# Kernel tuning notes

Measured on AMD Instinct MI355X. Metric: run time of the kernel, lower is better.

## Reference

```python
import jax, jax.numpy as jnp
import numpy as np

GROUPS = 16
N_HEADS = 4
EPS = 1e-6


def setup_inputs() -> dict:
    key = jax.random.key(0)
    ks = jax.random.split(key, 7)
    N, C, D, H, W = 2, 256, 16, 16, 16
    x = jax.random.normal(ks[0], (N, C, D, H, W), jnp.float32)
    gn_scale = 1.0 + 0.02 * jax.random.normal(ks[1], (C,), jnp.float32)
    gn_bias = 0.02 * jax.random.normal(ks[2], (C,), jnp.float32)
    w_qkv = jax.random.normal(ks[3], (3 * C, C), jnp.float32) / np.sqrt(C).astype(np.float32)
    b_qkv = 0.02 * jax.random.normal(ks[4], (3 * C,), jnp.float32)
    # NOTE: original zero-inits w_out/b_out (zero_module); we use random values
    # so the kernel-correctness baseline is non-trivial. Same math.
    w_out = jax.random.normal(ks[5], (C, C), jnp.float32) / np.sqrt(C).astype(np.float32)
    b_out = 0.02 * jax.random.normal(ks[6], (C,), jnp.float32)
    return {"x": x, "gn_scale": gn_scale, "gn_bias": gn_bias,
            "w_qkv": w_qkv, "b_qkv": b_qkv, "w_out": w_out, "b_out": b_out}


def reference(x, gn_scale, gn_bias, w_qkv, b_qkv, w_out, b_out):
    N, C, D, H, W = x.shape
    L = D * H * W
    xf = x.reshape(N, C, L)
    # GroupNorm(16 groups, eps=1e-6, affine)
    xg = xf.reshape(N, GROUPS, C // GROUPS, L)
    mu = xg.mean(axis=(2, 3), keepdims=True)
    var = xg.var(axis=(2, 3), keepdims=True)
    xn = ((xg - mu) * jax.lax.rsqrt(var + EPS)).reshape(N, C, L)
    xn = xn * gn_scale[None, :, None] + gn_bias[None, :, None]
    # 1x1x1 Conv3d == channel matmul
    qkv = jnp.einsum('oc,ncl->nol', w_qkv, xn) + b_qkv[None, :, None]  # [N,3C,L]
    ch = C // N_HEADS
    qkv = qkv.reshape(N, 3, N_HEADS, ch, L)  # channel layout: (qkvs, head, ch)
    q, k, v = qkv[:, 0], qkv[:, 1], qkv[:, 2]  # each [N,heads,ch,L]
    scale = 1.0 / np.sqrt(np.sqrt(ch)).astype(np.float32)
    w = jnp.einsum('nhct,nhcs->nhts', q * scale, k * scale)  # [N,heads,L,L]
    w = jax.nn.softmax(w, axis=-1)
    a = jnp.einsum('nhts,nhcs->nhct', w, v).reshape(N, C, L)
    y = jnp.einsum('oc,ncl->nol', w_out, a) + b_out[None, :, None]
    return x + y.reshape(N, C, D, H, W)
```

## Files before the change

### kernel.cpp

```cpp
#include <hip/hip_runtime.h>

#define NB 2
#define CCH 256
#define LL 4096
#define NGRP 16
#define NHD 4
#define CHD 64
#define QR 768
#define SPLIT 4
#define TBLK 256

typedef __attribute__((ext_vector_type(8))) short short8;
typedef __attribute__((ext_vector_type(4))) float f32x4;
typedef __attribute__((ext_vector_type(4))) unsigned int uint32x4;

#define OFF_GP 64
#define OFF_BP 4224
#define OFF_WQ 5824
#define OFF_WO 202432
#define OFF_QT 235200
#define OFF_KT 1283776
#define OFF_V  2332352
#define OFF_PO 3380928
#define OFF_L  7575232
#define OFF_XT OFF_PO
#define OFF_AT OFF_QT

#define KSCALE 0.1803368801111204f

__device__ __forceinline__ unsigned short f2bf(float f) {
    unsigned int u = __builtin_bit_cast(unsigned int, f);
    u += 0x7fffu + ((u >> 16) & 1u);
    return (unsigned short)(u >> 16);
}
__device__ __forceinline__ float bf2f(unsigned short s) {
    unsigned int u = ((unsigned int)s) << 16;
    return __builtin_bit_cast(float, u);
}
__device__ __forceinline__ unsigned int cvtpk(float lo, float hi) {
    unsigned int r;
    asm("v_cvt_pk_bf16_f32 %0, %1, %2" : "=v"(r) : "v"(lo), "v"(hi));
    return r;
}

__device__ __forceinline__ void barrier_lds_only() {
    asm volatile("s_waitcnt lgkmcnt(0)" ::: "memory");
    __builtin_amdgcn_s_barrier();
    __builtin_amdgcn_sched_barrier(0);
}

__device__ __forceinline__ short8 build_pf(const f32x4 s_lo, const f32x4 s_hi) {
    unsigned int a0 = cvtpk(s_lo[0], s_lo[1]);
    unsigned int b0 = cvtpk(s_hi[0], s_hi[1]);
    unsigned int a1 = cvtpk(s_lo[2], s_lo[3]);
    unsigned int b1 = cvtpk(s_hi[2], s_hi[3]);
    asm("v_permlane32_swap_b32 %0, %1" : "+v"(a0), "+v"(b0));
    asm("v_permlane16_swap_b32 %0, %1" : "+v"(a0), "+v"(b0));
    asm("v_permlane32_swap_b32 %0, %1" : "+v"(a1), "+v"(b1));
    asm("v_permlane16_swap_b32 %0, %1" : "+v"(a1), "+v"(b1));
    uint32x4 w = {a0, a1, b0, b1};
    return __builtin_bit_cast(short8, w);
}

__device__ __forceinline__ void stage_tile(unsigned short* lt,
                                           const unsigned short* src,
                                           int srcStride, int tid) {
    #pragma unroll
    for (int p = 0; p < 4; p++) {
        const int r  = p * 16 + (tid >> 4);
        const int cb = (tid & 15) * 2;
        const unsigned short* s = src + (size_t)r * srcStride + cb * 8;
        short8 a = *(const short8*)(s);
        short8 b = *(const short8*)(s + 8);
        char* d = (char*)lt + r * 512;
        *(short8*)(d + (((cb    ) ^ (r & 15)) << 4)) = a;
        *(short8*)(d + (((cb + 1) ^ (r & 15)) << 4)) = b;
    }
}
__device__ __forceinline__ short8 ldsfrag(const unsigned short* lt, int row, int ch) {
    return *(const short8*)((const char*)lt + row * 512 + ((ch ^ (row & 15)) << 4));
}

__global__ __launch_bounds__(256)
void k_xtgn(const float* __restrict__ x, unsigned short* __restrict__ xt,
            float* __restrict__ ws) {
    const int l0 = blockIdx.x * 64, c0 = blockIdx.y * 64, n = blockIdx.z;
    __shared__ __align__(16) unsigned short lt[64 * 64];
    __shared__ float red[2][4][4];
    const int tid = threadIdx.x;
    const int cl = tid >> 4;
    const int ll = (tid & 15) << 2;
    float s1[4], s2[4];
    #pragma unroll
    for (int cc = 0; cc < 4; cc++) {
        const int c = cl + cc * 16;
        float4 v = *(const float4*)(x + (size_t)(n * CCH + c0 + c) * LL + l0 + ll);
        s1[cc] = (v.x + v.y) + (v.z + v.w);
        s2[cc] = (v.x * v.x + v.y * v.y) + (v.z * v.z + v.w * v.w);
        const float vv[4] = {v.x, v.y, v.z, v.w};
        #pragma unroll
        for (int j = 0; j < 4; j++) {
            const int l = ll + j;
            const int byte = l * 128 + ((((c >> 3) ^ (l & 7)) << 4) | ((c & 7) * 2));
            *(unsigned short*)((char*)lt + byte) = f2bf(vv[j]);
        }
    }
    #pragma unroll
    for (int cc = 0; cc < 4; cc++)
        #pragma unroll
        for (int off = 32; off; off >>= 1) {
            s1[cc] += __shfl_down(s1[cc], off);
            s2[cc] += __shfl_down(s2[cc], off);
        }
    if ((tid & 63) == 0) {
        const int w = tid >> 6;
        #pragma unroll
        for (int cc = 0; cc < 4; cc++) { red[0][w][cc] = s1[cc]; red[1][w][cc] = s2[cc]; }
    }
    __syncthreads();
    if (tid < 4) {
        const float a = red[0][0][tid] + red[0][1][tid] + red[0][2][tid] + red[0][3][tid];
        const float b = red[1][0][tid] + red[1][1][tid] + red[1][2][tid] + red[1][3][tid];
        const int g = n * NGRP + (c0 >> 4) + tid;
        ws[OFF_GP + (g * 64 + blockIdx.x) * 2]     = a;
        ws[OFF_GP + (g * 64 + blockIdx.x) * 2 + 1] = b;
    }
    const int lr = tid >> 2;
    const int ch = (tid & 3) << 4;
    unsigned short* dst = xt + ((size_t)n * LL + l0 + lr) * CCH + c0 + ch;
    const int b0 = lr * 128 + ((((ch >> 3)    ) ^ (lr & 7)) << 4);
    const int b1 = lr * 128 + ((((ch >> 3) + 1) ^ (lr & 7)) << 4);
    *(short8*)dst       = *(const short8*)((char*)lt + b0);
    *(short8*)(dst + 8) = *(const short8*)((char*)lt + b1);
}

__device__ __forceinline__ void load_stats(const float* __restrict__ ws,
                                           float* smu, float* srs) {
    if (threadIdx.x < 32) {
        float s1 = 0.f, s2 = 0.f;
        #pragma unroll 8
        for (int i = 0; i < 64; i++) {
            s1 += ws[OFF_GP + (threadIdx.x * 64 + i) * 2];
            s2 += ws[OFF_GP + (threadIdx.x * 64 + i) * 2 + 1];
        }
        const float inv = 1.f / (float)(16 * LL);
        float m = s1 * inv;
        float var = s2 * inv - m * m;
        smu[threadIdx.x] = m;
        srs[threadIdx.x] = rsqrtf(var + 1e-6f);
    }
    __syncthreads();
}

__global__ __launch_bounds__(256)
void k_bpw(const float* __restrict__ w_qkv, const float* __restrict__ w_out,
           const float* __restrict__ b_qkv, const float* __restrict__ gn_scale,
           const float* __restrict__ gn_bias, float* __restrict__ ws,
           unsigned short* __restrict__ wq, unsigned short* __restrict__ wo) {
    __shared__ float smu[32], srs[32];
    load_stats(ws, smu, srs);
    if (blockIdx.x < 448) {
        const int e = (blockIdx.x * 256 + threadIdx.x) * 4;
        if (e < NB * QR * CCH) {
            const int n = (e >= QR * CCH) ? 1 : 0;
            const int r = e - n * QR * CCH;
            const int o = r >> 8, c = r & 255;
            float4 w  = *(const float4*)(w_qkv + (size_t)o * CCH + c);
            float4 gs = *(const float4*)(gn_scale + c);
            const float rs = srs[n * NGRP + (c >> 4)];
            const float sc = (o < 256 ? KSCALE : 1.0f) * rs;
            ushort4 u;
            u.x = f2bf(w.x * gs.x * sc); u.y = f2bf(w.y * gs.y * sc);
            u.z = f2bf(w.z * gs.z * sc); u.w = f2bf(w.w * gs.w * sc);
            *(ushort4*)(wq + (size_t)n * QR * CCH + r) = u;
        } else {
            const int r = e - NB * QR * CCH;
            float4 w = *(const float4*)(w_out + r);
            ushort4 u;
            u.x = f2bf(w.x); u.y = f2bf(w.y); u.z = f2bf(w.z); u.w = f2bf(w.w);
            *(ushort4*)(wo + r) = u;
        }
    } else {
        const int oi = (blockIdx.x - 448) * 32 + (threadIdx.x >> 3);
        const int j  = threadIdx.x & 7;
        const int n = (oi >= QR) ? 1 : 0;
        const int o = oi - n * QR;
        const float* wr = w_qkv + (size_t)o * CCH + j * 32;
        const float* gsr = gn_scale + j * 32;
        const float* gbr = gn_bias + j * 32;
        float s = 0.f;
        #pragma unroll
        for (int c = 0; c < 32; c += 4) {
            float4 w  = *(const float4*)(wr + c);
            float4 gs = *(const float4*)(gsr + c);
            float4 gb = *(const float4*)(gbr + c);
            const int gidx = n * NGRP + ((j * 32 + c) >> 4);
            const float mu = smu[gidx], rs = srs[gidx];
            s += w.x * (gb.x - mu * rs * gs.x) + w.y * (gb.y - mu * rs * gs.y)
               + w.z * (gb.z - mu * rs * gs.z) + w.w * (gb.w - mu * rs * gs.w);
        }
        s += __shfl_down(s, 4);
        s += __shfl_down(s, 2);
        s += __shfl_down(s, 1);
        if (j == 0) ws[OFF_BP + oi] = (b_qkv[o] + s) * (o < 256 ? KSCALE : 1.0f);
    }
}

__global__ __launch_bounds__(256)
void k_qkv(const unsigned short* __restrict__ wq, const float* __restrict__ bp,
           const unsigned short* __restrict__ xt,
           unsigned short* __restrict__ qT, unsigned short* __restrict__ kT,
           unsigned short* __restrict__ vv) {
    const int l0 = blockIdx.x * 64, o0 = blockIdx.y * 64, n = blockIdx.z;
    const int tid = threadIdx.x, w = tid >> 6, r16 = tid & 15, g = (tid & 63) >> 4;
    __shared__ __align__(16) unsigned short lt[64 * 256];
    const unsigned short* xb = xt + (size_t)n * LL * CCH;
    const unsigned short* wb = wq + (size_t)n * QR * CCH;
    const bool isv = (o0 >= 512);

    stage_tile(lt, isv ? (xb + (size_t)l0 * CCH) : (wb + (size_t)o0 * CCH), CCH, tid);
    __syncthreads();

    f32x4 acc[4];
    #pragma unroll
    for (int i = 0; i < 4; i++) acc[i] = (f32x4){0.f, 0.f, 0.f, 0.f};

    if (!isv) {
        const unsigned short* xr = xb + (size_t)(l0 + w * 16 + r16) * CCH + g * 8;
        for (int kk = 0; kk < 8; kk++) {
            short8 xf = *(const short8*)(xr + kk * 32);
            #pragma unroll
            for (int af = 0; af < 4; af++) {
                short8 wf = ldsfrag(lt, af * 16 + r16, kk * 4 + g);
                acc[af] = __builtin_amdgcn_mfma_f32_16x16x32_bf16(wf, xf, acc[af], 0, 0, 0);
            }
        }
        const bool isq = (o0 < 256);
        const int h = (o0 >> 6) & 3;
        unsigned short* tb = (isq ? qT : kT) + ((size_t)n * NHD + h) * LL * CHD;
        const int t = l0 + w * 16 + r16;
        #pragma unroll
        for (int af = 0; af < 4; af++) {
            float4 bb = *(const float4*)(bp + n * QR + o0 + af * 16 + g * 4);
            ushort4 u;
            u.x = f2bf(acc[af][0] + bb.x); u.y = f2bf(acc[af][1] + bb.y);
            u.z = f2bf(acc[af][2] + bb.z); u.w = f2bf(acc[af][3] + bb.w);
            *(ushort4*)(tb + (size_t)t * CHD + af * 16 + g * 4) = u;
        }
    } else {
        const unsigned short* wr = wb + (size_t)(o0 + w * 16 + r16) * CCH + g * 8;
        for (int kk = 0; kk < 8; kk++) {
            short8 wf = *(const short8*)(wr + kk * 32);
            #pragma unroll
            for (int lb = 0; lb < 4; lb++) {
                short8 xf = ldsfrag(lt, lb * 16 + r16, kk * 4 + g);
                acc[lb] = __builtin_amdgcn_mfma_f32_16x16x32_bf16(xf, wf, acc[lb], 0, 0, 0);
            }
        }
        const int h = (o0 - 512) >> 6;
        const int o = o0 + w * 16 + r16;
        const float bb = bp[n * QR + o];
        unsigned short* vb = vv + ((size_t)n * NHD + h) * CHD * LL + (size_t)(o & 63) * LL;
        #pragma unroll
        for (int lb = 0; lb < 4; lb++) {
            ushort4 u;
            u.x = f2bf(acc[lb][0] + bb); u.y = f2bf(acc[lb][1] + bb);
            u.z = f2bf(acc[lb][2] + bb); u.w = f2bf(acc[lb][3] + bb);
            *(ushort4*)(vb + l0 + lb * 16 + g * 4) = u;
        }
    }
}

__global__ __launch_bounds__(256, 2)
void k_attn(const unsigned short* __restrict__ qT,
            const unsigned short* __restrict__ kT,
            const unsigned short* __restrict__ vv,
            unsigned short* __restrict__ po, float* __restrict__ pl) {
    const int t0 = blockIdx.x * TBLK;
    const int h  = blockIdx.y;
    const int n  = blockIdx.z >> 2;
    const int sp = blockIdx.z & 3;
    const int tid = threadIdx.x;
    const int w = tid >> 6, l = tid & 63, r16 = l & 15, g = l >> 4;

    const size_t nh = (size_t)n * NHD + h;
    const unsigned short* qb = qT + nh * LL * CHD;
    const unsigned short* kb = kT + nh * LL * CHD;
    const unsigned short* vb = vv + nh * CHD * LL;
    const int s_beg = sp * (LL / SPLIT);

    __shared__ __align__(16) unsigned short kvs[2][2][64 * 64];

    const int srow = tid >> 2;
    const int ss0  = (tid & 3) << 1;
    const unsigned short* ksrc = kb + (size_t)(s_beg + srow) * CHD + ss0 * 8;
    const unsigned short* vsrc = vb + (size_t)srow * LL + s_beg + ss0 * 8;
    char* base0 = (char*)&kvs[0][0][0];
    const int kd0 = srow * 128 + (((ss0    ) ^ (srow & 7)) << 4);
    const int kd1 = srow * 128 + (((ss0 + 1) ^ (srow & 7)) << 4);

    const int tw = t0 + w * 64;
    const int jk0 = ((g    ) ^ (r16 & 7)) << 4;
    const int jk1 = ((4 + g) ^ (r16 & 7)) << 4;

    short8 ones;
    #pragma unroll
    for (int i = 0; i < 8; i++) ones[i] = (short)0x3F80;

    short8 qf[4][2];
    #pragma unroll
    for (int qg = 0; qg < 4; qg++) {
        const unsigned short* qr = qb + (size_t)(tw + qg * 16 + r16) * CHD + g * 8;
        qf[qg][0] = *(const short8*)(qr);
        qf[qg][1] = *(const short8*)(qr + 32);
    }

    f32x4 oacc[4][4], lacc[4];
    #pragma unroll
    for (int qg = 0; qg < 4; qg++) {
        lacc[qg] = (f32x4){0.f, 0.f, 0.f, 0.f};
        #pragma unroll
        for (int cb = 0; cb < 4; cb++) oacc[qg][cb] = (f32x4){0.f, 0.f, 0.f, 0.f};
    }

    const int NIT = (LL / SPLIT) / 64;

    short8 kr0 = *(const short8*)(ksrc);
    short8 kr1 = *(const short8*)(ksrc + 8);
    short8 vr0 = *(const short8*)(vsrc);
    short8 vr1 = *(const short8*)(vsrc + 8);
    *(short8*)(base0 + kd0) = kr0;
    *(short8*)(base0 + kd1) = kr1;
    *(short8*)(base0 + 8192 + kd0) = vr0;
    *(short8*)(base0 + 8192 + kd1) = vr1;
    const unsigned short* kpf = ksrc + 64 * CHD;
    const unsigned short* vpf = vsrc + 64;
    kr0 = *(const short8*)(kpf);
    kr1 = *(const short8*)(kpf + 8);
    vr0 = *(const short8*)(vpf);
    vr1 = *(const short8*)(vpf + 8);
    barrier_lds_only();

    int cur = 0;
    for (int it = 0; it < NIT; it++) {
        const char* kB = base0 + cur * 16384;
        const char* vB = kB + 8192;

        short8 kf0[4], kf1[4];
        #pragma unroll
        for (int sb = 0; sb < 4; sb++) {
            const int rb = (16 * sb + r16) * 128;
            kf0[sb] = *(const short8*)(kB + rb + jk0);
            kf1[sb] = *(const short8*)(kB + rb + jk1);
        }
        if (it + 1 < NIT) {
            char* kdn = base0 + (cur ^ 1) * 16384;
            *(short8*)(kdn + kd0) = kr0;
            *(short8*)(kdn + kd1) = kr1;
            *(short8*)(kdn + 8192 + kd0) = vr0;
            *(short8*)(kdn + 8192 + kd1) = vr1;
        }
        if (it + 2 < NIT) {
            kpf += 64 * CHD;
            vpf += 64;
            kr0 = *(const short8*)(kpf);
            kr1 = *(const short8*)(kpf + 8);
            vr0 = *(const short8*)(vpf);
            vr1 = *(const short8*)(vpf + 8);
        }

        short8 pf[4][2];
        #pragma unroll
        for (int qg = 0; qg < 4; qg++) {
            f32x4 sa[4];
            #pragma unroll
            for (int sb = 0; sb < 4; sb++) {
                f32x4 z = (f32x4){0.f, 0.f, 0.f, 0.f};
                z = __builtin_amdgcn_mfma_f32_16x16x32_bf16(kf0[sb], qf[qg][0], z, 0, 0, 0);
                sa[sb] = __builtin_amdgcn_mfma_f32_16x16x32_bf16(kf1[sb], qf[qg][1], z, 0, 0, 0);
            }
            #pragma unroll
            for (int sb = 0; sb < 4; sb++) {
                sa[sb][0] = __builtin_amdgcn_exp2f(sa[sb][0]);
                sa[sb][1] = __builtin_amdgcn_exp2f(sa[sb][1]);
                sa[sb][2] = __builtin_amdgcn_exp2f(sa[sb][2]);
                sa[sb][3] = __builtin_amdgcn_exp2f(sa[sb][3]);
            }
            pf[qg][0] = build_pf(sa[0], sa[1]);
            pf[qg][1] = build_pf(sa[2], sa[3]);
        }

        __builtin_amdgcn_s_setprio(1);
        #pragma unroll
        for (int cb = 0; cb < 4; cb++) {
            const int rb = (16 * cb + r16) * 128;
            short8 vf0 = *(const short8*)(vB + rb + jk0);
            short8 vf1 = *(const short8*)(vB + rb + jk1);
            #pragma unroll
            for (int qg = 0; qg < 4; qg++) {
                oacc[qg][cb] = __builtin_amdgcn_mfma_f32_16x16x32_bf16(vf0, pf[qg][0], oacc[qg][cb], 0, 0, 0);
                oacc[qg][cb] = __builtin_amdgcn_mfma_f32_16x16x32_bf16(vf1, pf[qg][1], oacc[qg][cb], 0, 0, 0);
            }
        }
        #pragma unroll
        for (int qg = 0; qg < 4; qg++) {
            lacc[qg] = __builtin_amdgcn_mfma_f32_16x16x32_bf16(ones, pf[qg][0], lacc[qg], 0, 0, 0);
            lacc[qg] = __builtin_amdgcn_mfma_f32_16x16x32_bf16(ones, pf[qg][1], lacc[qg], 0, 0, 0);
        }
        __builtin_amdgcn_s_setprio(0);

        barrier_lds_only();
        cur ^= 1;
    }

    const size_t nhsp = ((size_t)sp * NB + n) * NHD + h;
    #pragma unroll
    for (int qg = 0; qg < 4; qg++) {
        const int t = tw + qg * 16 + r16;
        unsigned short* pob = po + ((size_t)nhsp * LL + t) * CHD;
        #pragma unroll
        for (int cb = 0; cb < 4; cb++) {
            unsigned int lo = cvtpk(oacc[qg][cb][0], oacc[qg][cb][1]);
            unsigned int hi = cvtpk(oacc[qg][cb][2], oacc[qg][cb][3]);
            *(uint2*)(pob + cb * 16 + g * 4) = make_uint2(lo, hi);
        }
        if (g == 0) pl[nhsp * LL + t] = lacc[qg][0];
    }
}

__global__ __launch_bounds__(256)
void k_merge(const unsigned short* __restrict__ po, const float* __restrict__ pl,
             unsigned short* __restrict__ at) {
    const int idx = blockIdx.x * 256 + threadIdx.x;
    const int c16 = (idx & 3) << 4;
    const int t   = (idx >> 2) & (LL - 1);
    const int nh  = idx >> 14;
    float denom = 0.f;
    #pragma unroll
    for (int s = 0; s < SPLIT; s++)
        denom += pl[(size_t)(s * NB * NHD + nh) * LL + t];
    const float inv = 1.f / denom;
    float facc[16];
    #pragma unroll
    for (int k = 0; k < 16; k++) facc[k] = 0.f;
    #pragma unroll
    for (int s = 0; s < SPLIT; s++) {
        const unsigned short* pb = po + ((size_t)(s * NB * NHD + nh) * LL + t) * CHD + c16;
        short8 a = *(const short8*)(pb);
        short8 b = *(const short8*)(pb + 8);
        #pragma unroll
        for (int k = 0; k < 8; k++) {
            facc[k]     += bf2f((unsigned short)a[k]);
            facc[8 + k] += bf2f((unsigned short)b[k]);
        }
    }
    unsigned short* ob = at + ((size_t)(nh >> 2) * LL + t) * CCH + (nh & 3) * CHD + c16;
    #pragma unroll
    for (int q = 0; q < 4; q++) {
        ushort4 u;
        u.x = f2bf(facc[q * 4 + 0] * inv);
        u.y = f2bf(facc[q * 4 + 1] * inv);
        u.z = f2bf(facc[q * 4 + 2] * inv);
        u.w = f2bf(facc[q * 4 + 3] * inv);
        *(ushort4*)(ob + q * 4) = u;
    }
}

__global__ __launch_bounds__(256)
void k_out(const unsigned short* __restrict__ at, const unsigned short* __restrict__ wo,
           const float* __restrict__ b_out, const float* __restrict__ x,
           float* __restrict__ out) {
    const int l0 = blockIdx.x * 64, o0 = blockIdx.y * 64, n = blockIdx.z;
    const int tid = threadIdx.x, w = tid >> 6, r16 = tid & 15, g = (tid & 63) >> 4;
    __shared__ __align__(16) unsigned short lt[64 * 256];
    const unsigned short* ab = at + (size_t)n * LL * CCH;

    stage_tile(lt, ab + (size_t)l0 * CCH, CCH, tid);
    __syncthreads();

    const unsigned short* wr = wo + (size_t)(o0 + w * 16 + r16) * CCH + g * 8;
    f32x4 acc[4];
    #pragma unroll
    for (int i = 0; i < 4; i++) acc[i] = (f32x4){0.f, 0.f, 0.f, 0.f};
    for (int kk = 0; kk < 8; kk++) {
        short8 wf = *(const short8*)(wr + kk * 32);
        #pragma unroll
        for (int lb = 0; lb < 4; lb++) {
            short8 xf = ldsfrag(lt, lb * 16 + r16, kk * 4 + g);
            acc[lb] = __builtin_amdgcn_mfma_f32_16x16x32_bf16(xf, wf, acc[lb], 0, 0, 0);
        }
    }
    const int o = o0 + w * 16 + r16;
    const float bb = b_out[o];
    const float* xb = x + ((size_t)n * CCH + o) * LL;
    float* ob = out + ((size_t)n * CCH + o) * LL;
    #pragma unroll
    for (int lb = 0; lb < 4; lb++) {
        const int li = l0 + lb * 16 + g * 4;
        float4 xv = *(const float4*)(xb + li);
        float4 v;
        v.x = acc[lb][0] + bb + xv.x; v.y = acc[lb][1] + bb + xv.y;
        v.z = acc[lb][2] + bb + xv.z; v.w = acc[lb][3] + bb + xv.w;
        *(float4*)(ob + li) = v;
    }
}

extern "C" void kernel_launch(void* const* d_in, const int* in_sizes, int n_in,
                              void* d_out, int out_size, void* d_ws, size_t ws_size,
                              hipStream_t stream) {
    (void)in_sizes; (void)n_in; (void)out_size; (void)ws_size;
    const float* x        = (const float*)d_in[0];
    const float* gn_scale = (const float*)d_in[1];
    const float* gn_bias  = (const float*)d_in[2];
    const float* w_qkv    = (const float*)d_in[3];
    const float* b_qkv    = (const float*)d_in[4];
    const float* w_out    = (const float*)d_in[5];
    const float* b_out    = (const float*)d_in[6];
    float* out = (float*)d_out;
    float* ws  = (float*)d_ws;
    unsigned short* wq  = (unsigned short*)(ws + OFF_WQ);
    unsigned short* wo  = (unsigned short*)(ws + OFF_WO);
    unsigned short* xt  = (unsigned short*)(ws + OFF_XT);
    unsigned short* qT  = (unsigned short*)(ws + OFF_QT);
    unsigned short* kT  = (unsigned short*)(ws + OFF_KT);
    unsigned short* vv  = (unsigned short*)(ws + OFF_V);
    unsigned short* at  = (unsigned short*)(ws + OFF_AT);
    unsigned short* po  = (unsigned short*)(ws + OFF_PO);
    float* pl = ws + OFF_L;

    k_xtgn<<<dim3(64, 4, NB), 256, 0, stream>>>(x, xt, ws);
    k_bpw<<<dim3(496), 256, 0, stream>>>(w_qkv, w_out, b_qkv, gn_scale, gn_bias, ws, wq, wo);
    k_qkv<<<dim3(64, 12, NB), 256, 0, stream>>>(wq, ws + OFF_BP, xt, qT, kT, vv);
    k_attn<<<dim3(LL / TBLK, NHD, NB * SPLIT), 256, 0, stream>>>(qT, kT, vv, po, pl);
    k_merge<<<dim3(512), 256, 0, stream>>>(po, pl, at);
    k_out<<<dim3(64, 4, NB), 256, 0, stream>>>(at, wo, b_out, x, out);
}
```

Measured before the change: 79.22 us.

## Load K/V fragments straight from global in single-wave attention blocks

The attention kernel now launches one 64-thread wave per block instead of four waves sharing a double-buffered LDS K/V tile. Each wave reads its K and V MFMA fragments directly from global memory, and block indices are remapped so that blocks sharing a K/V slice are spread across XCDs. This removes LDS staging, barriers and the setprio hints in favour of relying on L2/cache reuse. In exchange it drops the explicit prefetch pipelining and may raise global-load traffic and exposed latency per wave.

```diff
diff --git a/kernel.cpp b/kernel.cpp
--- a/kernel.cpp
+++ b/kernel.cpp
@@ -8,7 +8,6 @@
 #define CHD 64
 #define QR 768
 #define SPLIT 4
-#define TBLK 256
 
 typedef __attribute__((ext_vector_type(8))) short short8;
 typedef __attribute__((ext_vector_type(4))) float f32x4;
@@ -41,12 +40,6 @@
     unsigned int r;
     asm("v_cvt_pk_bf16_f32 %0, %1, %2" : "=v"(r) : "v"(lo), "v"(hi));
     return r;
-}
-
-__device__ __forceinline__ void barrier_lds_only() {
-    asm volatile("s_waitcnt lgkmcnt(0)" ::: "memory");
-    __builtin_amdgcn_s_barrier();
-    __builtin_amdgcn_sched_barrier(0);
 }
 
 __device__ __forceinline__ short8 build_pf(const f32x4 s_lo, const f32x4 s_hi) {
@@ -271,17 +264,20 @@
     }
 }
 
-__global__ __launch_bounds__(256, 2)
+__global__ __launch_bounds__(64, 2)
 void k_attn(const unsigned short* __restrict__ qT,
             const unsigned short* __restrict__ kT,
             const unsigned short* __restrict__ vv,
             unsigned short* __restrict__ po, float* __restrict__ pl) {
-    const int t0 = blockIdx.x * TBLK;
-    const int h  = blockIdx.y;
-    const int n  = blockIdx.z >> 2;
-    const int sp = blockIdx.z & 3;
-    const int tid = threadIdx.x;
-    const int w = tid >> 6, l = tid & 63, r16 = l & 15, g = l >> 4;
+    const int flat = blockIdx.x;
+    const int orig = (flat & 7) * 256 + (flat >> 3);
+    const int tw = (orig & 63) * 64;
+    const int h  = (orig >> 6) & 3;
+    const int z  = orig >> 8;
+    const int n  = z >> 2;
+    const int sp = z & 3;
+    const int l  = threadIdx.x;
+    const int r16 = l & 15, g = l >> 4;
 
     const size_t nh = (size_t)n * NHD + h;
     const unsigned short* qb = qT + nh * LL * CHD;
@@ -289,19 +285,8 @@
     const unsigned short* vb = vv + nh * CHD * LL;
     const int s_beg = sp * (LL / SPLIT);
 
-    __shared__ __align__(16) unsigned short kvs[2][2][64 * 64];
-
-    const int srow = tid >> 2;
-    const int ss0  = (tid & 3) << 1;
-    const unsigned short* ksrc = kb + (size_t)(s_beg + srow) * CHD + ss0 * 8;
-    const unsigned short* vsrc = vb + (size_t)srow * LL + s_beg + ss0 * 8;
-    char* base0 = (char*)&kvs[0][0][0];
-    const int kd0 = srow * 128 + (((ss0    ) ^ (srow & 7)) << 4);
-    const int kd1 = srow * 128 + (((ss0 + 1) ^ (srow & 7)) << 4);
-
-    const int tw = t0 + w * 64;
-    const int jk0 = ((g    ) ^ (r16 & 7)) << 4;
-    const int jk1 = ((4 + g) ^ (r16 & 7)) << 4;
+    const unsigned short* ka = kb + (size_t)(s_beg + r16) * CHD + g * 8;
+    const unsigned short* va = vb + (size_t)r16 * LL + s_beg + g * 8;
 
     short8 ones;
     #pragma unroll
@@ -323,50 +308,20 @@
         for (int cb = 0; cb < 4; cb++) oacc[qg][cb] = (f32x4){0.f, 0.f, 0.f, 0.f};
     }
 
-    const int NIT = (LL / SPLIT) / 64;
-
-    short8 kr0 = *(const short8*)(ksrc);
-    short8 kr1 = *(const short8*)(ksrc + 8);
-    short8 vr0 = *(const short8*)(vsrc);
-    short8 vr1 = *(const short8*)(vsrc + 8);
-    *(short8*)(base0 + kd0) = kr0;
-    *(short8*)(base0 + kd1) = kr1;
-    *(short8*)(base0 + 8192 + kd0) = vr0;
-    *(short8*)(base0 + 8192 + kd1) = vr1;
-    const unsigned short* kpf = ksrc + 64 * CHD;
-    const unsigned short* vpf = vsrc + 64;
-    kr0 = *(const short8*)(kpf);
-    kr1 = *(const short8*)(kpf + 8);
-    vr0 = *(const short8*)(vpf);
-    vr1 = *(const short8*)(vpf + 8);
-    barrier_lds_only();
-
-    int cur = 0;
-    for (int it = 0; it < NIT; it++) {
-        const char* kB = base0 + cur * 16384;
-        const char* vB = kB + 8192;
-
+    for (int it = 0; it < (LL / SPLIT) / 64; it++) {
         short8 kf0[4], kf1[4];
         #pragma unroll
         for (int sb = 0; sb < 4; sb++) {
-            const int rb = (16 * sb + r16) * 128;
-            kf0[sb] = *(const short8*)(kB + rb + jk0);
-            kf1[sb] = *(const short8*)(kB + rb + jk1);
-        }
-        if (it + 1 < NIT) {
-            char* kdn = base0 + (cur ^ 1) * 16384;
-            *(short8*)(kdn + kd0) = kr0;
-            *(short8*)(kdn + kd1) = kr1;
-            *(short8*)(kdn + 8192 + kd0) = vr0;
-            *(short8*)(kdn + 8192 + kd1) = vr1;
-        }
-        if (it + 2 < NIT) {
-            kpf += 64 * CHD;
-            vpf += 64;
-            kr0 = *(const short8*)(kpf);
-            kr1 = *(const short8*)(kpf + 8);
-            vr0 = *(const short8*)(vpf);
-            vr1 = *(const short8*)(vpf + 8);
+            const unsigned short* kr = ka + (size_t)(it * 64 + sb * 16) * CHD;
+            kf0[sb] = *(const short8*)(kr);
+            kf1[sb] = *(const short8*)(kr + 32);
+        }
+        short8 vf0[4], vf1[4];
+        #pragma unroll
+        for (int cb = 0; cb < 4; cb++) {
+            const unsigned short* vr = va + (size_t)cb * 16 * LL + it * 64;
+            vf0[cb] = *(const short8*)(vr);
+            vf1[cb] = *(const short8*)(vr + 32);
         }
 
         short8 pf[4][2];
@@ -375,9 +330,9 @@
             f32x4 sa[4];
             #pragma unroll
             for (int sb = 0; sb < 4; sb++) {
-                f32x4 z = (f32x4){0.f, 0.f, 0.f, 0.f};
-                z = __builtin_amdgcn_mfma_f32_16x16x32_bf16(kf0[sb], qf[qg][0], z, 0, 0, 0);
-                sa[sb] = __builtin_amdgcn_mfma_f32_16x16x32_bf16(kf1[sb], qf[qg][1], z, 0, 0, 0);
+                f32x4 z4 = (f32x4){0.f, 0.f, 0.f, 0.f};
+                z4 = __builtin_amdgcn_mfma_f32_16x16x32_bf16(kf0[sb], qf[qg][0], z4, 0, 0, 0);
+                sa[sb] = __builtin_amdgcn_mfma_f32_16x16x32_bf16(kf1[sb], qf[qg][1], z4, 0, 0, 0);
             }
             #pragma unroll
             for (int sb = 0; sb < 4; sb++) {
@@ -390,16 +345,12 @@
             pf[qg][1] = build_pf(sa[2], sa[3]);
         }
 
-        __builtin_amdgcn_s_setprio(1);
         #pragma unroll
         for (int cb = 0; cb < 4; cb++) {
-            const int rb = (16 * cb + r16) * 128;
-            short8 vf0 = *(const short8*)(vB + rb + jk0);
-            short8 vf1 = *(const short8*)(vB + rb + jk1);
             #pragma unroll
             for (int qg = 0; qg < 4; qg++) {
-                oacc[qg][cb] = __builtin_amdgcn_mfma_f32_16x16x32_bf16(vf0, pf[qg][0], oacc[qg][cb], 0, 0, 0);
-                oacc[qg][cb] = __builtin_amdgcn_mfma_f32_16x16x32_bf16(vf1, pf[qg][1], oacc[qg][cb], 0, 0, 0);
+                oacc[qg][cb] = __builtin_amdgcn_mfma_f32_16x16x32_bf16(vf0[cb], pf[qg][0], oacc[qg][cb], 0, 0, 0);
+                oacc[qg][cb] = __builtin_amdgcn_mfma_f32_16x16x32_bf16(vf1[cb], pf[qg][1], oacc[qg][cb], 0, 0, 0);
             }
         }
         #pragma unroll
@@ -407,10 +358,6 @@
             lacc[qg] = __builtin_amdgcn_mfma_f32_16x16x32_bf16(ones, pf[qg][0], lacc[qg], 0, 0, 0);
             lacc[qg] = __builtin_amdgcn_mfma_f32_16x16x32_bf16(ones, pf[qg][1], lacc[qg], 0, 0, 0);
         }
-        __builtin_amdgcn_s_setprio(0);
-
-        barrier_lds_only();
-        cur ^= 1;
     }
 
     const size_t nhsp = ((size_t)sp * NB + n) * NHD + h;
@@ -531,7 +478,7 @@
     k_xtgn<<<dim3(64, 4, NB), 256, 0, stream>>>(x, xt, ws);
     k_bpw<<<dim3(496), 256, 0, stream>>>(w_qkv, w_out, b_qkv, gn_scale, gn_bias, ws, wq, wo);
     k_qkv<<<dim3(64, 12, NB), 256, 0, stream>>>(wq, ws + OFF_BP, xt, qT, kT, vv);
-    k_attn<<<dim3(LL / TBLK, NHD, NB * SPLIT), 256, 0, stream>>>(qT, kT, vv, po, pl);
+    k_attn<<<dim3(2048), 64, 0, stream>>>(qT, kT, vv, po, pl);
     k_merge<<<dim3(512), 256, 0, stream>>>(po, pl, at);
     k_out<<<dim3(64, 4, NB), 256, 0, stream>>>(at, wo, b_out, x, out);
 }
```

New measurement: 107.3 us. 1.35x slower.
